# Performance work log

Hardware: AMD Instinct MI355X
Metric: run time of the kernel (lower is better)

Reference implementation:

```python
import jax, jax.numpy as jnp
import numpy as np


def _bce_logits(x, z):
    # numerically stable binary_cross_entropy_with_logits (elementwise)
    return jnp.maximum(x, 0.0) - x * z + jnp.log1p(jnp.exp(-jnp.abs(x)))


def _giou(b1, b2):
    # boxes in (cx, cy, w, h) format, mirrors bbox_iou(..., mode='giou')
    eps = 1e-9
    b1x1 = b1[..., 0] - b1[..., 2] / 2; b1y1 = b1[..., 1] - b1[..., 3] / 2
    b1x2 = b1[..., 0] + b1[..., 2] / 2; b1y2 = b1[..., 1] + b1[..., 3] / 2
    b2x1 = b2[..., 0] - b2[..., 2] / 2; b2y1 = b2[..., 1] - b2[..., 3] / 2
    b2x2 = b2[..., 0] + b2[..., 2] / 2; b2y2 = b2[..., 1] + b2[..., 3] / 2
    a1 = jnp.clip(b1x2 - b1x1, 0.0) * jnp.clip(b1y2 - b1y1, 0.0) + eps
    a2 = jnp.clip(b2x2 - b2x1, 0.0) * jnp.clip(b2y2 - b2y1, 0.0) + eps
    iw = jnp.clip(jnp.minimum(b1x2, b2x2) - jnp.maximum(b1x1, b2x1), 0.0)
    ih = jnp.clip(jnp.minimum(b1y2, b2y2) - jnp.maximum(b1y1, b2y1), 0.0)
    inter = iw * ih + eps
    union = a1 + a2 - inter + eps
    iou = inter / union
    cw = jnp.maximum(b1x2, b2x2) - jnp.minimum(b1x1, b2x1)
    ch = jnp.maximum(b1y2, b2y2) - jnp.minimum(b1y1, b2y1)
    carea = cw * ch + eps
    return iou - (carea - union) / carea


def setup_inputs() -> dict:
    key = jax.random.key(0)
    ks = jax.random.split(key, 8)
    N, A, S, nC, nM, G, H, W = 4, 3, 13, 80, 32, 16, 104, 104
    preds = jax.random.normal(ks[0], (N, A, S, S, 5 + nC + nM), jnp.float32) * 0.5
    prototypes = jax.random.normal(ks[1], (N, nM, H, W), jnp.float32)
    masks = (jax.random.uniform(ks[2], (N, G, H, W)) < 0.3).astype(jnp.float32)
    ii = jnp.arange(S)
    interior = (ii >= 2) & (ii <= 10)
    int2d = interior[:, None] & interior[None, :]
    obj = (jax.random.uniform(ks[3], (N, A, S, S)) < 0.06) & int2d
    obj = obj.at[:, 0, 6, 6].set(True)  # guarantee >= 1 object per image
    xy = jax.random.uniform(ks[4], (N, A, S, S, 2), minval=0.2, maxval=0.8)
    wh = jax.random.uniform(ks[5], (N, A, S, S, 2), minval=0.5, maxval=2.5)
    cls = jax.random.randint(ks[6], (N, A, S, S, 1), 0, nC).astype(jnp.float32)
    mid = jax.random.randint(ks[7], (N, A, S, S, 1), 0, G).astype(jnp.float32)
    target = jnp.concatenate([xy, wh, obj[..., None].astype(jnp.float32), cls, mid], axis=-1)
    anchors = jnp.array([[1.0, 1.5], [2.0, 2.5], [3.5, 3.0]], jnp.float32)
    return {"preds": preds, "target": target, "anchors": anchors,
            "prototypes": prototypes, "masks": masks,
            "num_classes": 80, "num_masks": 32}


def reference(preds, target, anchors, prototypes, masks, num_classes, num_masks):
    eps = 1e-9
    N, A, S = preds.shape[0], preds.shape[1], preds.shape[2]
    H, W = prototypes.shape[2], prototypes.shape[3]
    nC, nM = num_classes, num_masks
    dt = preds.dtype
    conf_t = target[..., 4]
    obj = conf_t == 1.0
    noobj = conf_t == 0.0
    objf = obj.astype(dt)
    noobjf = noobj.astype(dt)
    n_obj = objf.sum()
    n_noobj = noobjf.sum()
    conf_logit = preds[..., 4]
    noobj_loss = (_bce_logits(conf_logit, conf_t) * noobjf).sum() / n_noobj
    # ---- segmentation loss (dense masked equivalent of ragged per-instance crops) ----
    coeffs = jnp.tanh(preds[..., 5 + nC:5 + nC + nM])            # [N,A,S,S,M]
    inst = jnp.einsum('naijm,nmhw->naijhw', coeffs, prototypes)   # instance logits
    cols = jnp.arange(S, dtype=dt)
    # cells_to_boxes: normalized image coords, then scaled to prototype pixels
    bx = (target[..., 0] + cols[None, None, None, :]) / S * W
    by = (target[..., 1] + cols[None, None, :, None]) / S * H
    bw = target[..., 2] / S * W
    bh = target[..., 3] / S * H
    x1 = jnp.floor(bx - bw / 2).astype(jnp.int32)
    x2 = jnp.floor(bx + bw / 2).astype(jnp.int32)
    y1 = jnp.floor(by - bh / 2).astype(jnp.int32)
    y2 = jnp.floor(by + bh / 2).astype(jnp.int32)
    ids = jnp.clip(target[..., 6].astype(jnp.int32), 0, masks.shape[1] - 1)
    tm = masks[jnp.arange(N)[:, None, None, None], ids]           # [N,A,S,S,H,W]
    hh = jnp.arange(H)
    ww = jnp.arange(W)
    rm = ((hh >= y1[..., None]) & (hh < y2[..., None])).astype(dt)  # [N,A,S,S,H]
    cm = ((ww >= x1[..., None]) & (ww < x2[..., None])).astype(dt)  # [N,A,S,S,W]
    bce_el = _bce_logits(inst, tm)
    region_sum = jnp.einsum('naijhw,naijh,naijw->naij', bce_el, rm, cm)
    area = rm.sum(-1) * cm.sum(-1)
    valid = (area > 0) & obj
    seg_mean = jnp.where(valid, region_sum / jnp.maximum(area, 1.0), 0.0)
    segment_loss = seg_mean.sum() / (valid.astype(dt).sum() + eps)
    # ---- box / obj / class losses ----
    anch = anchors.reshape(1, A, 1, 1, 2)
    pred_box = jnp.concatenate([jax.nn.sigmoid(preds[..., 0:2]),
                                jnp.exp(preds[..., 2:4]) * anch], axis=-1)
    giou = _giou(pred_box, target[..., 0:4])                      # [N,A,S,S]
    obj_tgt = conf_t * jnp.clip(jax.lax.stop_gradient(giou), 0.0)
    obj_loss = (_bce_logits(conf_logit, obj_tgt) * objf).sum() / n_obj
    # note: original applies BCEWithLogits to sigmoid(xy) (double squash) - faithful
    xy_bce = (_bce_logits(jax.nn.sigmoid(preds[..., 0:2]), target[..., 0:2])
              * objf[..., None]).sum() / (n_obj * 2)
    twh = jnp.log(1e-16 + target[..., 2:4] / anch)
    wh_mse = (((preds[..., 2:4] - twh) ** 2) * objf[..., None]).sum() / (n_obj * 2)
    box_loss = xy_bce + wh_mse + ((1.0 - giou) * objf).sum() / n_obj
    logp = jax.nn.log_softmax(preds[..., 5:5 + nC], axis=-1)
    labels = target[..., 5].astype(jnp.int32)
    nll = -jnp.take_along_axis(logp, labels[..., None], axis=-1)[..., 0]
    class_loss = (nll * objf).sum() / n_obj
    box_l = 8.0 * box_loss
    obj_l = 2.0 * obj_loss
    noobj_l = 4.0 * noobj_loss
    cls_l = 1.0 * class_loss
    seg_l = 10.0 * segment_loss
    total = box_l + obj_l + noobj_l + cls_l + seg_l
    return jnp.stack([box_l, obj_l, noobj_l, cls_l, seg_l, total])
```

## Files before the change

kernel.cpp:

```cpp
#include <hip/hip_runtime.h>
#include <math.h>

#define N_  4
#define A_  3
#define S_  13
#define NC_ 80
#define NM_ 32
#define G_  16
#define H_  104
#define W_  104
#define CH_ (5 + NC_ + NM_)
#define HW_ (H_ * W_)

#define STR 32

__device__ __forceinline__ float bce_logits(float x, float z) {
    return fmaxf(x, 0.0f) - x * z + log1pf(expf(-fabsf(x)));
}

__device__ __forceinline__ float sigmoidf(float x) {
    return 1.0f / (1.0f + expf(-x));
}

__device__ __forceinline__ float giou_fn(float cx1, float cy1, float w1, float h1,
                                         float cx2, float cy2, float w2, float h2) {
    const float eps = 1e-9f;
    float b1x1 = cx1 - w1 * 0.5f, b1y1 = cy1 - h1 * 0.5f;
    float b1x2 = cx1 + w1 * 0.5f, b1y2 = cy1 + h1 * 0.5f;
    float b2x1 = cx2 - w2 * 0.5f, b2y1 = cy2 - h2 * 0.5f;
    float b2x2 = cx2 + w2 * 0.5f, b2y2 = cy2 + h2 * 0.5f;
    float a1 = fmaxf(b1x2 - b1x1, 0.0f) * fmaxf(b1y2 - b1y1, 0.0f) + eps;
    float a2 = fmaxf(b2x2 - b2x1, 0.0f) * fmaxf(b2y2 - b2y1, 0.0f) + eps;
    float iw = fmaxf(fminf(b1x2, b2x2) - fmaxf(b1x1, b2x1), 0.0f);
    float ih = fmaxf(fminf(b1y2, b2y2) - fmaxf(b1y1, b2y1), 0.0f);
    float inter = iw * ih + eps;
    float uni   = a1 + a2 - inter + eps;
    float iou   = inter / uni;
    float cw = fmaxf(b1x2, b2x2) - fminf(b1x1, b2x1);
    float ch = fmaxf(b1y2, b2y2) - fminf(b1y1, b2y1);
    float carea = cw * ch + eps;
    return iou - (carea - uni) / carea;
}

__global__ __launch_bounds__(256) void yolo_cell_kernel(
    const float* __restrict__ preds,
    const float* __restrict__ target,
    const float* __restrict__ anchors,
    const float* __restrict__ protos,
    const float* __restrict__ masks,
    float* __restrict__ acc)
{
    const int cell = blockIdx.x;
    const int j = cell % S_;
    const int i = (cell / S_) % S_;
    const int a = (cell / (S_ * S_)) % A_;
    const int n = cell / (A_ * S_ * S_);
    const int tid = threadIdx.x;

    const float* p = preds  + (size_t)cell * CH_;
    const float* t = target + (size_t)cell * 7;

    __shared__ float s_tc[NM_];
    __shared__ float s_red[256];

    const float conf_t = t[4];
    const bool obj = (conf_t == 1.0f);

    if (tid == 0) {
        float x = p[4];
        if (conf_t == 0.0f) {
            atomicAdd(&acc[1 * STR], 1.0f);
            atomicAdd(&acc[2 * STR], bce_logits(x, 0.0f));
        }
        if (obj) {
            float tx = t[0], ty = t[1], tw = t[2], th = t[3];
            float aw = anchors[a * 2 + 0], ah = anchors[a * 2 + 1];
            float sx = sigmoidf(p[0]);
            float sy = sigmoidf(p[1]);
            float pw = expf(p[2]) * aw;
            float ph = expf(p[3]) * ah;
            float giou = giou_fn(sx, sy, pw, ph, tx, ty, tw, th);
            atomicAdd(&acc[0 * STR], 1.0f);
            atomicAdd(&acc[3 * STR], bce_logits(x, fmaxf(giou, 0.0f)));
            atomicAdd(&acc[4 * STR], bce_logits(sx, tx) + bce_logits(sy, ty));
            float twl = logf(1e-16f + tw / aw);
            float thl = logf(1e-16f + th / ah);
            float dw = p[2] - twl, dh = p[3] - thl;
            atomicAdd(&acc[5 * STR], dw * dw + dh * dh);
            atomicAdd(&acc[6 * STR], 1.0f - giou);
        }
    }

    if (obj && tid >= 64 && tid < 128) {
        int lane = tid - 64;
        float v0 = (lane      < NC_) ? p[5 + lane]      : -1e30f;
        float v1 = (lane + 64 < NC_) ? p[5 + lane + 64] : -1e30f;
        float mx = fmaxf(v0, v1);
        for (int o = 32; o > 0; o >>= 1) mx = fmaxf(mx, __shfl_xor(mx, o, 64));
        float se = ((lane      < NC_) ? expf(v0 - mx) : 0.0f)
                 + ((lane + 64 < NC_) ? expf(v1 - mx) : 0.0f);
        for (int o = 32; o > 0; o >>= 1) se += __shfl_xor(se, o, 64);
        if (lane == 0) {
            int label = (int)t[5];
            float lse = mx + logf(se);
            atomicAdd(&acc[7 * STR], lse - p[5 + label]);
        }
    }

    if (obj) {
        float tx = t[0], ty = t[1], tw = t[2], th = t[3];
        float bx = (tx + (float)j) * ((float)W_ / (float)S_);
        float by = (ty + (float)i) * ((float)H_ / (float)S_);
        float bw = tw * ((float)W_ / (float)S_);
        float bh = th * ((float)H_ / (float)S_);
        int x1 = (int)floorf(bx - bw * 0.5f);
        int x2 = (int)floorf(bx + bw * 0.5f);
        int y1 = (int)floorf(by - bh * 0.5f);
        int y2 = (int)floorf(by + bh * 0.5f);
        int lox = max(x1, 0), hix = min(x2, W_);
        int loy = max(y1, 0), hiy = min(y2, H_);
        int ncols = max(hix - lox, 0);
        int nrows = max(hiy - loy, 0);
        int area = nrows * ncols;

        if (tid < NM_) s_tc[tid] = tanhf(p[5 + NC_ + tid]);
        __syncthreads();

        float lsum = 0.0f;
        if (area > 0) {
            int id = (int)t[6];
            id = min(max(id, 0), G_ - 1);
            const float* tm = masks  + ((size_t)(n * G_ + id)) * HW_;
            const float* pr = protos + (size_t)n * NM_ * HW_;
            for (int px = tid; px < area; px += 256) {
                int h = loy + px / ncols;
                int w = lox + px % ncols;
                int off = h * W_ + w;
                float inst = 0.0f;
#pragma unroll
                for (int m = 0; m < NM_; ++m)
                    inst += s_tc[m] * pr[m * HW_ + off];
                lsum += bce_logits(inst, tm[off]);
            }
        }

        s_red[tid] = lsum;
        __syncthreads();
        for (int s = 128; s > 0; s >>= 1) {
            if (tid < s) s_red[tid] += s_red[tid + s];
            __syncthreads();
        }
        if (tid == 0 && area > 0) {
            float seg_mean = s_red[0] / fmaxf((float)area, 1.0f);
            atomicAdd(&acc[8 * STR], seg_mean);
            atomicAdd(&acc[9 * STR], 1.0f);
        }
    }
}

__global__ void yolo_finalize_kernel(const float* __restrict__ acc,
                                     float* __restrict__ out)
{
    if (threadIdx.x == 0 && blockIdx.x == 0) {
        float n_obj   = acc[0 * STR];
        float n_noobj = acc[1 * STR];
        float noobj_loss = acc[2 * STR] / n_noobj;
        float obj_loss   = acc[3 * STR] / n_obj;
        float xy_bce     = acc[4 * STR] / (n_obj * 2.0f);
        float wh_mse     = acc[5 * STR] / (n_obj * 2.0f);
        float box_loss   = xy_bce + wh_mse + acc[6 * STR] / n_obj;
        float class_loss = acc[7 * STR] / n_obj;
        float seg_loss   = acc[8 * STR] / (acc[9 * STR] + 1e-9f);
        float box_l   = 8.0f * box_loss;
        float obj_l   = 2.0f * obj_loss;
        float noobj_l = 4.0f * noobj_loss;
        float cls_l   = 1.0f * class_loss;
        float seg_l   = 10.0f * seg_loss;
        out[0] = box_l;
        out[1] = obj_l;
        out[2] = noobj_l;
        out[3] = cls_l;
        out[4] = seg_l;
        out[5] = box_l + obj_l + noobj_l + cls_l + seg_l;
    }
}

extern "C" void kernel_launch(void* const* d_in, const int* in_sizes, int n_in,
                              void* d_out, int out_size, void* d_ws, size_t ws_size,
                              hipStream_t stream) {
    const float* preds   = (const float*)d_in[0];
    const float* target  = (const float*)d_in[1];
    const float* anchors = (const float*)d_in[2];
    const float* protos  = (const float*)d_in[3];
    const float* masks   = (const float*)d_in[4];

    float* acc = (float*)d_ws;
    float* out = (float*)d_out;

    hipMemsetAsync(d_ws, 0, 10 * STR * sizeof(float), stream);

    const int ncells = N_ * A_ * S_ * S_;
    yolo_cell_kernel<<<ncells, 256, 0, stream>>>(preds, target, anchors,
                                                 protos, masks, acc);
    yolo_finalize_kernel<<<1, 64, 0, stream>>>(acc, out);
}
```

Before: 101.7 us.

## Split cell loss into per-thread pass plus compacted segmentation kernel

```diff
diff --git a/kernel.cpp b/kernel.cpp
--- a/kernel.cpp
+++ b/kernel.cpp
@@ -11,6 +11,7 @@
 #define W_  104
 #define CH_ (5 + NC_ + NM_)
 #define HW_ (H_ * W_)
+#define NCELL (N_ * A_ * S_ * S_)
 
 #define STR 32
 
@@ -46,33 +47,33 @@
     const float* __restrict__ preds,
     const float* __restrict__ target,
     const float* __restrict__ anchors,
-    const float* __restrict__ protos,
-    const float* __restrict__ masks,
-    float* __restrict__ acc)
+    float* __restrict__ acc,
+    int* __restrict__ valid_cnt,
+    int* __restrict__ valid_list)
 {
-    const int cell = blockIdx.x;
-    const int j = cell % S_;
-    const int i = (cell / S_) % S_;
-    const int a = (cell / (S_ * S_)) % A_;
-    const int n = cell / (A_ * S_ * S_);
-    const int tid = threadIdx.x;
-
-    const float* p = preds  + (size_t)cell * CH_;
-    const float* t = target + (size_t)cell * 7;
-
-    __shared__ float s_tc[NM_];
-    __shared__ float s_red[256];
-
-    const float conf_t = t[4];
-    const bool obj = (conf_t == 1.0f);
-
-    if (tid == 0) {
-        float x = p[4];
+    const int tid  = threadIdx.x;
+    const int cell = blockIdx.x * 256 + tid;
+    const bool active = (cell < NCELL);
+
+    float v_nobj = 0.0f, v_nnoobj = 0.0f, v_noobjbce = 0.0f, v_objbce = 0.0f;
+    float v_xy = 0.0f, v_wh = 0.0f, v_g = 0.0f, v_nll = 0.0f;
+
+    if (active) {
+        const int j = cell % S_;
+        const int i = (cell / S_) % S_;
+        const int a = (cell / (S_ * S_)) % A_;
+
+        const float* t = target + (size_t)cell * 7;
+        const float* p = preds  + (size_t)cell * CH_;
+
+        const float conf_t = t[4];
+        const float x = p[4];
+
         if (conf_t == 0.0f) {
-            atomicAdd(&acc[1 * STR], 1.0f);
-            atomicAdd(&acc[2 * STR], bce_logits(x, 0.0f));
-        }
-        if (obj) {
+            v_nnoobj   = 1.0f;
+            v_noobjbce = bce_logits(x, 0.0f);
+        } else if (conf_t == 1.0f) {
+            v_nobj = 1.0f;
             float tx = t[0], ty = t[1], tw = t[2], th = t[3];
             float aw = anchors[a * 2 + 0], ah = anchors[a * 2 + 1];
             float sx = sigmoidf(p[0]);
@@ -80,34 +81,86 @@
             float pw = expf(p[2]) * aw;
             float ph = expf(p[3]) * ah;
             float giou = giou_fn(sx, sy, pw, ph, tx, ty, tw, th);
-            atomicAdd(&acc[0 * STR], 1.0f);
-            atomicAdd(&acc[3 * STR], bce_logits(x, fmaxf(giou, 0.0f)));
-            atomicAdd(&acc[4 * STR], bce_logits(sx, tx) + bce_logits(sy, ty));
+            v_objbce = bce_logits(x, fmaxf(giou, 0.0f));
+            v_xy     = bce_logits(sx, tx) + bce_logits(sy, ty);
             float twl = logf(1e-16f + tw / aw);
             float thl = logf(1e-16f + th / ah);
             float dw = p[2] - twl, dh = p[3] - thl;
-            atomicAdd(&acc[5 * STR], dw * dw + dh * dh);
-            atomicAdd(&acc[6 * STR], 1.0f - giou);
+            v_wh = dw * dw + dh * dh;
+            v_g  = 1.0f - giou;
+
+            float mx = -1e30f;
+            #pragma unroll 8
+            for (int c = 0; c < NC_; ++c) mx = fmaxf(mx, p[5 + c]);
+            float se = 0.0f;
+            #pragma unroll 8
+            for (int c = 0; c < NC_; ++c) se += expf(p[5 + c] - mx);
+            int label = (int)t[5];
+            v_nll = (mx + logf(se)) - p[5 + label];
+
+            float bx = (tx + (float)j) * ((float)W_ / (float)S_);
+            float by = (ty + (float)i) * ((float)H_ / (float)S_);
+            float bw = tw * ((float)W_ / (float)S_);
+            float bh = th * ((float)H_ / (float)S_);
+            int x1 = (int)floorf(bx - bw * 0.5f);
+            int x2 = (int)floorf(bx + bw * 0.5f);
+            int y1 = (int)floorf(by - bh * 0.5f);
+            int y2 = (int)floorf(by + bh * 0.5f);
+            int ncols = max(min(x2, W_) - max(x1, 0), 0);
+            int nrows = max(min(y2, H_) - max(y1, 0), 0);
+            if (nrows * ncols > 0) {
+                int slot = atomicAdd(valid_cnt, 1);
+                valid_list[slot] = cell;
+            }
         }
     }
 
-    if (obj && tid >= 64 && tid < 128) {
-        int lane = tid - 64;
-        float v0 = (lane      < NC_) ? p[5 + lane]      : -1e30f;
-        float v1 = (lane + 64 < NC_) ? p[5 + lane + 64] : -1e30f;
-        float mx = fmaxf(v0, v1);
-        for (int o = 32; o > 0; o >>= 1) mx = fmaxf(mx, __shfl_xor(mx, o, 64));
-        float se = ((lane      < NC_) ? expf(v0 - mx) : 0.0f)
-                 + ((lane + 64 < NC_) ? expf(v1 - mx) : 0.0f);
-        for (int o = 32; o > 0; o >>= 1) se += __shfl_xor(se, o, 64);
-        if (lane == 0) {
-            int label = (int)t[5];
-            float lse = mx + logf(se);
-            atomicAdd(&acc[7 * STR], lse - p[5 + label]);
-        }
-    }
-
-    if (obj) {
+    #pragma unroll
+    for (int o = 32; o > 0; o >>= 1) {
+        v_nobj     += __shfl_xor(v_nobj,     o, 64);
+        v_nnoobj   += __shfl_xor(v_nnoobj,   o, 64);
+        v_noobjbce += __shfl_xor(v_noobjbce, o, 64);
+        v_objbce   += __shfl_xor(v_objbce,   o, 64);
+        v_xy       += __shfl_xor(v_xy,       o, 64);
+        v_wh       += __shfl_xor(v_wh,       o, 64);
+        v_g        += __shfl_xor(v_g,        o, 64);
+        v_nll      += __shfl_xor(v_nll,      o, 64);
+    }
+    if ((tid & 63) == 0) {
+        atomicAdd(&acc[0 * STR], v_nobj);
+        atomicAdd(&acc[1 * STR], v_nnoobj);
+        atomicAdd(&acc[2 * STR], v_noobjbce);
+        atomicAdd(&acc[3 * STR], v_objbce);
+        atomicAdd(&acc[4 * STR], v_xy);
+        atomicAdd(&acc[5 * STR], v_wh);
+        atomicAdd(&acc[6 * STR], v_g);
+        atomicAdd(&acc[7 * STR], v_nll);
+    }
+}
+
+#define SEG_BLOCKS 64
+__global__ __launch_bounds__(256) void yolo_seg_kernel(
+    const float* __restrict__ preds,
+    const float* __restrict__ target,
+    const float* __restrict__ protos,
+    const float* __restrict__ masks,
+    const int* __restrict__ valid_cnt,
+    const int* __restrict__ valid_list,
+    float* __restrict__ acc)
+{
+    __shared__ float s_tc[NM_];
+    __shared__ float s_red[4];
+    const int tid = threadIdx.x;
+    const int count = *valid_cnt;
+
+    for (int idx = blockIdx.x; idx < count; idx += SEG_BLOCKS) {
+        const int cell = valid_list[idx];
+        const int j = cell % S_;
+        const int i = (cell / S_) % S_;
+        const int n = cell / (A_ * S_ * S_);
+        const float* t = target + (size_t)cell * 7;
+        const float* p = preds  + (size_t)cell * CH_;
+
         float tx = t[0], ty = t[1], tw = t[2], th = t[3];
         float bx = (tx + (float)j) * ((float)W_ / (float)S_);
         float by = (ty + (float)i) * ((float)H_ / (float)S_);
@@ -119,46 +172,43 @@
         int y2 = (int)floorf(by + bh * 0.5f);
         int lox = max(x1, 0), hix = min(x2, W_);
         int loy = max(y1, 0), hiy = min(y2, H_);
-        int ncols = max(hix - lox, 0);
-        int nrows = max(hiy - loy, 0);
-        int area = nrows * ncols;
+        int ncols = hix - lox;
+        int area  = (hiy - loy) * ncols;
 
         if (tid < NM_) s_tc[tid] = tanhf(p[5 + NC_ + tid]);
         __syncthreads();
 
+        int id = (int)t[6];
+        id = min(max(id, 0), G_ - 1);
+        const float* tm = masks  + ((size_t)(n * G_ + id)) * HW_;
+        const float* pr = protos + (size_t)n * NM_ * HW_;
+
         float lsum = 0.0f;
-        if (area > 0) {
-            int id = (int)t[6];
-            id = min(max(id, 0), G_ - 1);
-            const float* tm = masks  + ((size_t)(n * G_ + id)) * HW_;
-            const float* pr = protos + (size_t)n * NM_ * HW_;
-            for (int px = tid; px < area; px += 256) {
-                int h = loy + px / ncols;
-                int w = lox + px % ncols;
-                int off = h * W_ + w;
-                float inst = 0.0f;
-#pragma unroll
-                for (int m = 0; m < NM_; ++m)
-                    inst += s_tc[m] * pr[m * HW_ + off];
-                lsum += bce_logits(inst, tm[off]);
-            }
+        for (int px = tid; px < area; px += 256) {
+            int h = loy + px / ncols;
+            int w = lox + px % ncols;
+            int off = h * W_ + w;
+            float inst = 0.0f;
+            #pragma unroll
+            for (int m = 0; m < NM_; ++m)
+                inst += s_tc[m] * pr[m * HW_ + off];
+            lsum += bce_logits(inst, tm[off]);
         }
 
-        s_red[tid] = lsum;
+        #pragma unroll
+        for (int o = 32; o > 0; o >>= 1) lsum += __shfl_xor(lsum, o, 64);
+        if ((tid & 63) == 0) s_red[tid >> 6] = lsum;
         __syncthreads();
-        for (int s = 128; s > 0; s >>= 1) {
-            if (tid < s) s_red[tid] += s_red[tid + s];
-            __syncthreads();
+        if (tid == 0) {
+            float tot = s_red[0] + s_red[1] + s_red[2] + s_red[3];
+            atomicAdd(&acc[8 * STR], tot / fmaxf((float)area, 1.0f));
         }
-        if (tid == 0 && area > 0) {
-            float seg_mean = s_red[0] / fmaxf((float)area, 1.0f);
-            atomicAdd(&acc[8 * STR], seg_mean);
-            atomicAdd(&acc[9 * STR], 1.0f);
-        }
+        __syncthreads();
     }
 }
 
 __global__ void yolo_finalize_kernel(const float* __restrict__ acc,
+                                     const int* __restrict__ valid_cnt,
                                      float* __restrict__ out)
 {
     if (threadIdx.x == 0 && blockIdx.x == 0) {
@@ -170,7 +220,8 @@
         float wh_mse     = acc[5 * STR] / (n_obj * 2.0f);
         float box_loss   = xy_bce + wh_mse + acc[6 * STR] / n_obj;
         float class_loss = acc[7 * STR] / n_obj;
-        float seg_loss   = acc[8 * STR] / (acc[9 * STR] + 1e-9f);
+        float n_valid    = (float)(*valid_cnt);
+        float seg_loss   = acc[8 * STR] / (n_valid + 1e-9f);
         float box_l   = 8.0f * box_loss;
         float obj_l   = 2.0f * obj_loss;
         float noobj_l = 4.0f * noobj_loss;
@@ -194,13 +245,17 @@
     const float* protos  = (const float*)d_in[3];
     const float* masks   = (const float*)d_in[4];
 
-    float* acc = (float*)d_ws;
-    float* out = (float*)d_out;
-
-    hipMemsetAsync(d_ws, 0, 10 * STR * sizeof(float), stream);
-
-    const int ncells = N_ * A_ * S_ * S_;
-    yolo_cell_kernel<<<ncells, 256, 0, stream>>>(preds, target, anchors,
-                                                 protos, masks, acc);
-    yolo_finalize_kernel<<<1, 64, 0, stream>>>(acc, out);
-}
+    float* acc       = (float*)d_ws;
+    int*   valid_cnt = (int*)((char*)d_ws + 10 * STR * sizeof(float));
+    int*   valid_list= (int*)((char*)d_ws + 11 * STR * sizeof(float));
+    float* out       = (float*)d_out;
+
+    hipMemsetAsync(d_ws, 0, 11 * STR * sizeof(float), stream);
+
+    const int ablocks = (NCELL + 255) / 256;
+    yolo_cell_kernel<<<ablocks, 256, 0, stream>>>(preds, target, anchors,
+                                                  acc, valid_cnt, valid_list);
+    yolo_seg_kernel<<<SEG_BLOCKS, 256, 0, stream>>>(preds, target, protos, masks,
+                                                    valid_cnt, valid_list, acc);
+    yolo_finalize_kernel<<<1, 64, 0, stream>>>(acc, valid_cnt, out);
+}
```

New measurement: 100.7 us. Within noise of the previous version (-1.0%).

## Replace per-cell atomics with fixed 64-block partial sums and compacted object lists

Applied to the files above, without the earlier changes.

```diff
diff --git a/kernel.cpp b/kernel.cpp
--- a/kernel.cpp
+++ b/kernel.cpp
@@ -11,8 +11,10 @@
 #define W_  104
 #define CH_ (5 + NC_ + NM_)
 #define HW_ (H_ * W_)
-
-#define STR 32
+#define NCELL (N_ * A_ * S_ * S_)
+
+#define MAIN_BLOCKS 64
+#define PROW 16
 
 __device__ __forceinline__ float bce_logits(float x, float z) {
     return fmaxf(x, 0.0f) - x * z + log1pf(expf(-fabsf(x)));
@@ -42,135 +44,206 @@
     return iou - (carea - uni) / carea;
 }
 
-__global__ __launch_bounds__(256) void yolo_cell_kernel(
+__device__ __forceinline__ int region_bounds(const float* t, int i, int j,
+                                             int& lox, int& loy, int& ncols, int& nrows) {
+    float bx = (t[0] + (float)j) * ((float)W_ / (float)S_);
+    float by = (t[1] + (float)i) * ((float)H_ / (float)S_);
+    float bw = t[2] * ((float)W_ / (float)S_);
+    float bh = t[3] * ((float)H_ / (float)S_);
+    int x1 = (int)floorf(bx - bw * 0.5f);
+    int x2 = (int)floorf(bx + bw * 0.5f);
+    int y1 = (int)floorf(by - bh * 0.5f);
+    int y2 = (int)floorf(by + bh * 0.5f);
+    lox = max(x1, 0); loy = max(y1, 0);
+    ncols = max(min(x2, W_) - lox, 0);
+    nrows = max(min(y2, H_) - loy, 0);
+    return nrows * ncols;
+}
+
+__global__ __launch_bounds__(256) void yolo_main_kernel(
     const float* __restrict__ preds,
     const float* __restrict__ target,
     const float* __restrict__ anchors,
     const float* __restrict__ protos,
     const float* __restrict__ masks,
-    float* __restrict__ acc)
+    float* __restrict__ partials)
 {
-    const int cell = blockIdx.x;
-    const int j = cell % S_;
-    const int i = (cell / S_) % S_;
-    const int a = (cell / (S_ * S_)) % A_;
-    const int n = cell / (A_ * S_ * S_);
+    const int b   = blockIdx.x;
     const int tid = threadIdx.x;
 
-    const float* p = preds  + (size_t)cell * CH_;
-    const float* t = target + (size_t)cell * 7;
-
     __shared__ float s_tc[NM_];
-    __shared__ float s_red[256];
-
-    const float conf_t = t[4];
-    const bool obj = (conf_t == 1.0f);
+    __shared__ float s_w[4][8];
+    __shared__ float s_red[4];
+    __shared__ int   s_list[40];
+    __shared__ int   s_nvalid;
+
+    if (b < 8) {
+        const int cell = b * 256 + tid;
+        float v0 = 0.f, v1 = 0.f, v2 = 0.f, v3 = 0.f,
+              v4 = 0.f, v5 = 0.f, v6 = 0.f, v7 = 0.f;
+
+        if (cell < NCELL) {
+            const int a = (cell / (S_ * S_)) % A_;
+            const float* t = target + (size_t)cell * 7;
+            const float* p = preds  + (size_t)cell * CH_;
+            const float conf_t = t[4];
+            const float x = p[4];
+
+            if (conf_t == 0.0f) {
+                v1 = 1.0f;
+                v2 = bce_logits(x, 0.0f);
+            } else if (conf_t == 1.0f) {
+                v0 = 1.0f;
+                float tx = t[0], ty = t[1], tw = t[2], th = t[3];
+                float aw = anchors[a * 2 + 0], ah = anchors[a * 2 + 1];
+                float sx = sigmoidf(p[0]);
+                float sy = sigmoidf(p[1]);
+                float pw = expf(p[2]) * aw;
+                float ph = expf(p[3]) * ah;
+                float giou = giou_fn(sx, sy, pw, ph, tx, ty, tw, th);
+                v3 = bce_logits(x, fmaxf(giou, 0.0f));
+                v4 = bce_logits(sx, tx) + bce_logits(sy, ty);
+                float twl = logf(1e-16f + tw / aw);
+                float thl = logf(1e-16f + th / ah);
+                float dw = p[2] - twl, dh = p[3] - thl;
+                v5 = dw * dw + dh * dh;
+                v6 = 1.0f - giou;
+
+                float mx = -1e30f;
+                #pragma unroll 8
+                for (int c = 0; c < NC_; ++c) mx = fmaxf(mx, p[5 + c]);
+                float se = 0.0f;
+                #pragma unroll 8
+                for (int c = 0; c < NC_; ++c) se += expf(p[5 + c] - mx);
+                int label = (int)t[5];
+                v7 = (mx + logf(se)) - p[5 + label];
+            }
+        }
+
+        #pragma unroll
+        for (int o = 32; o > 0; o >>= 1) {
+            v0 += __shfl_xor(v0, o, 64);  v1 += __shfl_xor(v1, o, 64);
+            v2 += __shfl_xor(v2, o, 64);  v3 += __shfl_xor(v3, o, 64);
+            v4 += __shfl_xor(v4, o, 64);  v5 += __shfl_xor(v5, o, 64);
+            v6 += __shfl_xor(v6, o, 64);  v7 += __shfl_xor(v7, o, 64);
+        }
+        if ((tid & 63) == 0) {
+            int w = tid >> 6;
+            s_w[w][0] = v0; s_w[w][1] = v1; s_w[w][2] = v2; s_w[w][3] = v3;
+            s_w[w][4] = v4; s_w[w][5] = v5; s_w[w][6] = v6; s_w[w][7] = v7;
+        }
+        __syncthreads();
+        if (tid < 8) {
+            partials[b * PROW + tid] =
+                s_w[0][tid] + s_w[1][tid] + s_w[2][tid] + s_w[3][tid];
+        }
+        __syncthreads();
+    }
+
+    if (tid == 0) s_nvalid = 0;
+    __syncthreads();
+    if (tid < 32) {
+        int c = tid * 64 + b;
+        if (c < NCELL) {
+            const float* t = target + (size_t)c * 7;
+            if (t[4] == 1.0f) {
+                int lox, loy, ncols, nrows;
+                int area = region_bounds(t, (c / S_) % S_, c % S_,
+                                         lox, loy, ncols, nrows);
+                if (area > 0) {
+                    int k = atomicAdd(&s_nvalid, 1);
+                    s_list[k] = c;
+                }
+            }
+        }
+    }
+    __syncthreads();
+    const int nv = s_nvalid;
+    float block_seg = 0.0f;
+
+    for (int ii = 0; ii < nv; ++ii) {
+        const int cell = s_list[ii];
+        const int j = cell % S_;
+        const int i = (cell / S_) % S_;
+        const int n = cell / (A_ * S_ * S_);
+        const float* t = target + (size_t)cell * 7;
+        const float* p = preds  + (size_t)cell * CH_;
+
+        int lox, loy, ncols, nrows;
+        int area = region_bounds(t, i, j, lox, loy, ncols, nrows);
+
+        if (tid < NM_) s_tc[tid] = tanhf(p[5 + NC_ + tid]);
+        __syncthreads();
+
+        int id = (int)t[6];
+        id = min(max(id, 0), G_ - 1);
+        const float* tm = masks  + ((size_t)(n * G_ + id)) * HW_;
+        const float* pr = protos + (size_t)n * NM_ * HW_;
+
+        float lsum = 0.0f;
+        for (int px = tid; px < area; px += 256) {
+            int h = loy + px / ncols;
+            int w = lox + px % ncols;
+            int off = h * W_ + w;
+            float inst = 0.0f;
+            #pragma unroll
+            for (int m = 0; m < NM_; ++m)
+                inst += s_tc[m] * pr[m * HW_ + off];
+            lsum += bce_logits(inst, tm[off]);
+        }
+
+        #pragma unroll
+        for (int o = 32; o > 0; o >>= 1) lsum += __shfl_xor(lsum, o, 64);
+        if ((tid & 63) == 0) s_red[tid >> 6] = lsum;
+        __syncthreads();
+        if (tid == 0) {
+            float tot = s_red[0] + s_red[1] + s_red[2] + s_red[3];
+            block_seg += tot / fmaxf((float)area, 1.0f);
+        }
+        __syncthreads();
+    }
 
     if (tid == 0) {
-        float x = p[4];
-        if (conf_t == 0.0f) {
-            atomicAdd(&acc[1 * STR], 1.0f);
-            atomicAdd(&acc[2 * STR], bce_logits(x, 0.0f));
-        }
-        if (obj) {
-            float tx = t[0], ty = t[1], tw = t[2], th = t[3];
-            float aw = anchors[a * 2 + 0], ah = anchors[a * 2 + 1];
-            float sx = sigmoidf(p[0]);
-            float sy = sigmoidf(p[1]);
-            float pw = expf(p[2]) * aw;
-            float ph = expf(p[3]) * ah;
-            float giou = giou_fn(sx, sy, pw, ph, tx, ty, tw, th);
-            atomicAdd(&acc[0 * STR], 1.0f);
-            atomicAdd(&acc[3 * STR], bce_logits(x, fmaxf(giou, 0.0f)));
-            atomicAdd(&acc[4 * STR], bce_logits(sx, tx) + bce_logits(sy, ty));
-            float twl = logf(1e-16f + tw / aw);
-            float thl = logf(1e-16f + th / ah);
-            float dw = p[2] - twl, dh = p[3] - thl;
-            atomicAdd(&acc[5 * STR], dw * dw + dh * dh);
-            atomicAdd(&acc[6 * STR], 1.0f - giou);
-        }
-    }
-
-    if (obj && tid >= 64 && tid < 128) {
-        int lane = tid - 64;
-        float v0 = (lane      < NC_) ? p[5 + lane]      : -1e30f;
-        float v1 = (lane + 64 < NC_) ? p[5 + lane + 64] : -1e30f;
-        float mx = fmaxf(v0, v1);
-        for (int o = 32; o > 0; o >>= 1) mx = fmaxf(mx, __shfl_xor(mx, o, 64));
-        float se = ((lane      < NC_) ? expf(v0 - mx) : 0.0f)
-                 + ((lane + 64 < NC_) ? expf(v1 - mx) : 0.0f);
-        for (int o = 32; o > 0; o >>= 1) se += __shfl_xor(se, o, 64);
-        if (lane == 0) {
-            int label = (int)t[5];
-            float lse = mx + logf(se);
-            atomicAdd(&acc[7 * STR], lse - p[5 + label]);
-        }
-    }
-
-    if (obj) {
-        float tx = t[0], ty = t[1], tw = t[2], th = t[3];
-        float bx = (tx + (float)j) * ((float)W_ / (float)S_);
-        float by = (ty + (float)i) * ((float)H_ / (float)S_);
-        float bw = tw * ((float)W_ / (float)S_);
-        float bh = th * ((float)H_ / (float)S_);
-        int x1 = (int)floorf(bx - bw * 0.5f);
-        int x2 = (int)floorf(bx + bw * 0.5f);
-        int y1 = (int)floorf(by - bh * 0.5f);
-        int y2 = (int)floorf(by + bh * 0.5f);
-        int lox = max(x1, 0), hix = min(x2, W_);
-        int loy = max(y1, 0), hiy = min(y2, H_);
-        int ncols = max(hix - lox, 0);
-        int nrows = max(hiy - loy, 0);
-        int area = nrows * ncols;
-
-        if (tid < NM_) s_tc[tid] = tanhf(p[5 + NC_ + tid]);
-        __syncthreads();
-
-        float lsum = 0.0f;
-        if (area > 0) {
-            int id = (int)t[6];
-            id = min(max(id, 0), G_ - 1);
-            const float* tm = masks  + ((size_t)(n * G_ + id)) * HW_;
-            const float* pr = protos + (size_t)n * NM_ * HW_;
-            for (int px = tid; px < area; px += 256) {
-                int h = loy + px / ncols;
-                int w = lox + px % ncols;
-                int off = h * W_ + w;
-                float inst = 0.0f;
-#pragma unroll
-                for (int m = 0; m < NM_; ++m)
-                    inst += s_tc[m] * pr[m * HW_ + off];
-                lsum += bce_logits(inst, tm[off]);
-            }
-        }
-
-        s_red[tid] = lsum;
-        __syncthreads();
-        for (int s = 128; s > 0; s >>= 1) {
-            if (tid < s) s_red[tid] += s_red[tid + s];
-            __syncthreads();
-        }
-        if (tid == 0 && area > 0) {
-            float seg_mean = s_red[0] / fmaxf((float)area, 1.0f);
-            atomicAdd(&acc[8 * STR], seg_mean);
-            atomicAdd(&acc[9 * STR], 1.0f);
-        }
-    }
-}
-
-__global__ void yolo_finalize_kernel(const float* __restrict__ acc,
-                                     float* __restrict__ out)
+        partials[b * PROW + 8] = block_seg;
+        partials[b * PROW + 9] = (float)nv;
+    }
+}
+
+__global__ __launch_bounds__(64) void yolo_finalize_kernel(
+    const float* __restrict__ partials,
+    float* __restrict__ out)
 {
-    if (threadIdx.x == 0 && blockIdx.x == 0) {
-        float n_obj   = acc[0 * STR];
-        float n_noobj = acc[1 * STR];
-        float noobj_loss = acc[2 * STR] / n_noobj;
-        float obj_loss   = acc[3 * STR] / n_obj;
-        float xy_bce     = acc[4 * STR] / (n_obj * 2.0f);
-        float wh_mse     = acc[5 * STR] / (n_obj * 2.0f);
-        float box_loss   = xy_bce + wh_mse + acc[6 * STR] / n_obj;
-        float class_loss = acc[7 * STR] / n_obj;
-        float seg_loss   = acc[8 * STR] / (acc[9 * STR] + 1e-9f);
+    const int t = threadIdx.x;
+    float s0 = 0.f, s1 = 0.f, s2 = 0.f, s3 = 0.f,
+          s4 = 0.f, s5 = 0.f, s6 = 0.f, s7 = 0.f, s8 = 0.f, s9 = 0.f;
+    if (t < 8) {
+        s0 = partials[t * PROW + 0]; s1 = partials[t * PROW + 1];
+        s2 = partials[t * PROW + 2]; s3 = partials[t * PROW + 3];
+        s4 = partials[t * PROW + 4]; s5 = partials[t * PROW + 5];
+        s6 = partials[t * PROW + 6]; s7 = partials[t * PROW + 7];
+    }
+    s8 = partials[t * PROW + 8];
+    s9 = partials[t * PROW + 9];
+
+    #pragma unroll
+    for (int o = 32; o > 0; o >>= 1) {
+        s0 += __shfl_xor(s0, o, 64);  s1 += __shfl_xor(s1, o, 64);
+        s2 += __shfl_xor(s2, o, 64);  s3 += __shfl_xor(s3, o, 64);
+        s4 += __shfl_xor(s4, o, 64);  s5 += __shfl_xor(s5, o, 64);
+        s6 += __shfl_xor(s6, o, 64);  s7 += __shfl_xor(s7, o, 64);
+        s8 += __shfl_xor(s8, o, 64);  s9 += __shfl_xor(s9, o, 64);
+    }
+
+    if (t == 0) {
+        float n_obj   = s0;
+        float n_noobj = s1;
+        float noobj_loss = s2 / n_noobj;
+        float obj_loss   = s3 / n_obj;
+        float xy_bce     = s4 / (n_obj * 2.0f);
+        float wh_mse     = s5 / (n_obj * 2.0f);
+        float box_loss   = xy_bce + wh_mse + s6 / n_obj;
+        float class_loss = s7 / n_obj;
+        float seg_loss   = s8 / (s9 + 1e-9f);
         float box_l   = 8.0f * box_loss;
         float obj_l   = 2.0f * obj_loss;
         float noobj_l = 4.0f * noobj_loss;
@@ -194,13 +267,10 @@
     const float* protos  = (const float*)d_in[3];
     const float* masks   = (const float*)d_in[4];
 
-    float* acc = (float*)d_ws;
-    float* out = (float*)d_out;
-
-    hipMemsetAsync(d_ws, 0, 10 * STR * sizeof(float), stream);
-
-    const int ncells = N_ * A_ * S_ * S_;
-    yolo_cell_kernel<<<ncells, 256, 0, stream>>>(preds, target, anchors,
-                                                 protos, masks, acc);
-    yolo_finalize_kernel<<<1, 64, 0, stream>>>(acc, out);
-}
+    float* partials = (float*)d_ws;
+    float* out      = (float*)d_out;
+
+    yolo_main_kernel<<<MAIN_BLOCKS, 256, 0, stream>>>(preds, target, anchors,
+                                                      protos, masks, partials);
+    yolo_finalize_kernel<<<1, 64, 0, stream>>>(partials, out);
+}
```

Result: faster. 94.67 us (-6.9%).
